# Kernel tuning notes

Measured on AMD Instinct MI355X. Metric: run time of the kernel, lower is better.

## Reference

```python
import jax, jax.numpy as jnp
import numpy as np

N = 50000
E = 600000
IN_C = 128
HID_C = 128
OUT_C = 128


def _glorot(key, shape):
    fan_in, fan_out = shape[0], shape[1]
    lim = np.sqrt(6.0 / (fan_in + fan_out))
    return jax.random.uniform(key, shape, jnp.float32, -lim, lim)


def setup_inputs() -> dict:
    key = jax.random.key(0)
    ks = jax.random.split(key, 10)
    x = jax.random.normal(ks[0], (N, IN_C), jnp.float32)
    edge_index = jax.random.randint(ks[1], (2, E), 0, N, jnp.int64)
    return {
        "x": x,
        "edge_index": edge_index,
        # SAGEConv1: lin_l (aggregated, with bias) and lin_r (root, no bias)
        "W1_l": _glorot(ks[2], (IN_C, HID_C)),
        "b1_l": jnp.zeros((HID_C,), jnp.float32),
        "W1_r": _glorot(ks[3], (IN_C, HID_C)),
        # SAGEConv2
        "W2_l": _glorot(ks[4], (HID_C, OUT_C)),
        "b2_l": jnp.zeros((OUT_C,), jnp.float32),
        "W2_r": _glorot(ks[5], (HID_C, OUT_C)),
        # final Linear(hidden+out -> out)
        "W_lin": _glorot(ks[6], (HID_C + OUT_C, OUT_C)),
        "b_lin": jnp.zeros((OUT_C,), jnp.float32),
    }


def _sage_conv(x, src, dst, W_l, b_l, W_r):
    # mean-aggregate source features onto destination nodes
    msg = x[src]                                   # [E, C] gather
    agg = jax.ops.segment_sum(msg, dst, num_segments=N)        # [N, C]
    cnt = jax.ops.segment_sum(jnp.ones((src.shape[0],), x.dtype), dst,
                              num_segments=N)                   # [N]
    mean = agg / jnp.maximum(cnt, 1.0)[:, None]
    return mean @ W_l + b_l + x @ W_r


def reference(x, edge_index, W1_l, b1_l, W1_r, W2_l, b2_l, W2_r, W_lin, b_lin):
    src, dst = edge_index[0], edge_index[1]
    x1 = jax.nn.relu(_sage_conv(x, src, dst, W1_l, b1_l, W1_r))   # [N, HID]
    x2 = jax.nn.relu(_sage_conv(x1, src, dst, W2_l, b2_l, W2_r))  # [N, OUT]
    return jnp.concatenate([x1, x2], axis=-1) @ W_lin + b_lin     # [N, OUT]
```

## Files before the change

### kernel.cpp

```cpp
#include <hip/hip_runtime.h>


typedef _Float16 f16;
typedef unsigned int u32;
typedef __attribute__((ext_vector_type(4))) _Float16 f16x4;
typedef __attribute__((ext_vector_type(8))) _Float16 f16x8;
typedef __attribute__((ext_vector_type(4))) float f32x4;

#define RNB 128

__global__ void prep_kernel(const float* __restrict__ x, f16* __restrict__ xh, int n4,
                            const int* __restrict__ ei, int* __restrict__ ghist, int E,
                            const float* __restrict__ W1l, const float* __restrict__ W1r,
                            const float* __restrict__ W2l, const float* __restrict__ W2r,
                            const float* __restrict__ Wlin, f16* __restrict__ wt,
                            int cb, int wb) {
  int b = blockIdx.x;
  if (b < cb) {
    int i = b * 256 + threadIdx.x;
    if (i < n4) {
      const float4 v = ((const float4*)x)[i];
      f16x4 h = { (f16)v.x, (f16)v.y, (f16)v.z, (f16)v.w };
      ((f16x4*)xh)[i] = h;
    }
  } else if (b < cb + wb) {
    int tid = (b - cb) * 256 + threadIdx.x;
    int w = tid >> 15, idx = tid & 32767;
    int j = idx & 7, n = (idx >> 3) & 127, chunk = idx >> 10;
    int k = chunk * 8 + j;
    float v;
    if (w == 0) v = (k < 128) ? W1l[k * 128 + n] : W1r[(k - 128) * 128 + n];
    else if (w == 1) v = (k < 128) ? W2l[k * 128 + n] : W2r[(k - 128) * 128 + n];
    else v = Wlin[k * 128 + n];
    wt[tid] = (f16)v;
  } else {
    __shared__ int h[256];
    int tid = threadIdx.x, rb = b - cb - wb;
    h[tid] = 0;
    __syncthreads();
    int per = (E + RNB - 1) / RNB;
    int s = rb * per, e = s + per; if (e > E) e = E;
    for (int i = s + tid; i < e; i += 256) atomicAdd(&h[ei[E + i] >> 8], 1);
    __syncthreads();
    ghist[tid * RNB + rb] = h[tid];
  }
}

__device__ inline int block_excl_scan256(int v, int* ws) {
  int lane = threadIdx.x & 63, w = threadIdx.x >> 6;
  int incl = v;
#pragma unroll
  for (int o = 1; o < 64; o <<= 1) {
    int u = __shfl_up(incl, o);
    if (lane >= o) incl += u;
  }
  if (lane == 63) ws[w] = incl;
  __syncthreads();
  int base = 0;
#pragma unroll
  for (int i = 0; i < 4; ++i) base += (i < w) ? ws[i] : 0;
  return base + incl - v;
}

__global__ void radix_scatter(const int* __restrict__ ei, const int* __restrict__ ghist,
                              u32* __restrict__ tmp, int E) {
  __shared__ int cur[256];
  __shared__ int ws[4];
  int tid = threadIdx.x, b = blockIdx.x;
  const int* row = ghist + tid * RNB;
  int part = 0, rest = 0;
  for (int i = 0; i < b; ++i) part += row[i];
  for (int i = b; i < RNB; ++i) rest += row[i];
  int total = part + rest;
  int excl = block_excl_scan256(total, ws);
  cur[tid] = excl + part;
  __syncthreads();
  int per = (E + RNB - 1) / RNB;
  int s = b * per, e = s + per; if (e > E) e = E;
  for (int i = s + tid; i < e; i += 256) {
    int d = ei[E + i], sr = ei[i];
    int pos = atomicAdd(&cur[d >> 8], 1);
    tmp[pos] = ((u32)sr << 8) | (u32)(d & 255);
  }
}

__global__ void radix_bucket(const u32* __restrict__ tmp, const int* __restrict__ ghist,
                             int* __restrict__ srcs, int* __restrict__ off,
                             int N, int E, int HB) {
  __shared__ int h[256], sc[256], cur[256];
  __shared__ int bsc[257];
  __shared__ int ws[4];
  int tid = threadIdx.x, hb = blockIdx.x;
  const int* row = ghist + tid * RNB;
  int total = 0;
#pragma unroll 4
  for (int i = 0; i < RNB; ++i) total += row[i];
  int excl = block_excl_scan256(total, ws);
  bsc[tid] = excl;
  if (tid == 255) bsc[256] = E;
  h[tid] = 0;
  __syncthreads();
  int start = bsc[hb];
  int end = bsc[hb + 1];
  for (int i = start + tid; i < end; i += 256) atomicAdd(&h[tmp[i] & 255u], 1);
  __syncthreads();
  sc[tid] = h[tid];
  __syncthreads();
  for (int o = 1; o < 256; o <<= 1) {
    int u = (tid >= o) ? sc[tid - o] : 0;
    __syncthreads();
    sc[tid] += u;
    __syncthreads();
  }
  int exclb = sc[tid] - h[tid];
  int v = (hb << 8) + tid;
  if (v < N) off[v] = start + exclb;
  if (hb == 0 && tid == 0) off[N] = E;
  cur[tid] = start + exclb;
  __syncthreads();
  for (int i = start + tid; i < end; i += 256) {
    u32 p = tmp[i];
    int pos = atomicAdd(&cur[p & 255u], 1);
    srcs[pos] = (int)(p >> 8);
  }
}

#define AGG_R 6
template <bool HEAD>
__global__ __launch_bounds__(256, 4) void fused_kernel(
    const f16* __restrict__ feat,
    const int* __restrict__ off, const int* __restrict__ srcs,
    const f16* __restrict__ WtA, const f16* __restrict__ WtB,
    const float* __restrict__ bA, const float* __restrict__ bB,
    void* __restrict__ outp, int n) {
  __shared__ f16 lds[16384];
  int tid = threadIdx.x;
  int wave = tid >> 6, lane = tid & 63;
  int sub = lane >> 4, n15 = lane & 15;
  int base = blockIdx.x * 32;

#pragma unroll
  for (int i = 0; i < 4; ++i)
    ((f16x8*)lds)[i * 256 + tid] = ((const f16x8*)WtA)[i * 256 + tid];

#pragma unroll 1
  for (int p = 0; p < 4; ++p) {
    int ln0 = p * 8 + wave * 2;
    int w0 = base + ln0, w1 = w0 + 1;
    bool a0 = w0 < n, a1 = w1 < n;
    int beg0 = a0 ? off[w0] : 0;
    int end0 = a0 ? off[w0 + 1] : 0;
    int beg1 = end0;
    int end1 = a1 ? off[w1 + 1] : end0;
    int deg0 = end0 - beg0, deg1 = end1 - beg1;

    int s0[AGG_R], s1[AGG_R];
    bool v0[AGG_R], v1[AGG_R];
#pragma unroll
    for (int k = 0; k < AGG_R; ++k) {
      int pp = 4 * k + sub;
      v0[k] = pp < deg0;  s0[k] = v0[k] ? srcs[beg0 + pp] : 0;
      v1[k] = pp < deg1;  s1[k] = v1[k] ? srcs[beg1 + pp] : 0;
    }
    f16x8 g0[AGG_R], g1[AGG_R];
#pragma unroll
    for (int k = 0; k < AGG_R; ++k) {
      if (v0[k]) g0[k] = *(const f16x8*)(feat + (size_t)s0[k] * 128 + n15 * 8);
      if (v1[k]) g1[k] = *(const f16x8*)(feat + (size_t)s1[k] * 128 + n15 * 8);
    }
    float acc0[8] = {}, acc1[8] = {};
#pragma unroll
    for (int k = 0; k < AGG_R; ++k) {
      if (v0[k]) {
#pragma unroll
        for (int j = 0; j < 8; ++j) acc0[j] += (float)g0[k][j];
      }
      if (v1[k]) {
#pragma unroll
        for (int j = 0; j < 8; ++j) acc1[j] += (float)g1[k][j];
      }
    }
    for (int e = beg0 + 4 * AGG_R; e < end0; e += 4) {
      if (sub < end0 - e) {
        int s = srcs[e + sub];
        f16x8 g = *(const f16x8*)(feat + (size_t)s * 128 + n15 * 8);
#pragma unroll
        for (int j = 0; j < 8; ++j) acc0[j] += (float)g[j];
      }
    }
    for (int e = beg1 + 4 * AGG_R; e < end1; e += 4) {
      if (sub < end1 - e) {
        int s = srcs[e + sub];
        f16x8 g = *(const f16x8*)(feat + (size_t)s * 128 + n15 * 8);
#pragma unroll
        for (int j = 0; j < 8; ++j) acc1[j] += (float)g[j];
      }
    }
#pragma unroll
    for (int j = 0; j < 8; ++j) {
      acc0[j] += __shfl_xor(acc0[j], 16);
      acc0[j] += __shfl_xor(acc0[j], 32);
      acc1[j] += __shfl_xor(acc1[j], 16);
      acc1[j] += __shfl_xor(acc1[j], 32);
    }
    if (sub == 0) {
      float inv = 1.0f / fmaxf((float)deg0, 1.0f);
      f16x8 o;
#pragma unroll
      for (int j = 0; j < 8; ++j) o[j] = (f16)(acc0[j] * inv);
      *(f16x8*)(lds + 8192 + ln0 * 128 + ((n15 ^ (ln0 & 15)) << 3)) = o;
    } else if (sub == 1) {
      float inv = 1.0f / fmaxf((float)deg1, 1.0f);
      int ln1 = ln0 + 1;
      f16x8 o;
#pragma unroll
      for (int j = 0; j < 8; ++j) o[j] = (f16)(acc1[j] * inv);
      *(f16x8*)(lds + 8192 + ln1 * 128 + ((n15 ^ (ln1 & 15)) << 3)) = o;
    }
  }
  __syncthreads();

  int rg = wave & 1, ch = wave >> 1;
  int rowl = rg * 16 + n15;
  int colb = ch * 64;

  f16x8 a[8];
#pragma unroll
  for (int kk = 0; kk < 4; ++kk)
    a[kk] = *(const f16x8*)(lds + 8192 + rowl * 128 + (((kk * 4 + sub) ^ n15) << 3));
  {
    int node = base + rowl; if (node >= n) node = n - 1;
    const f16* bp = feat + (size_t)node * 128 + sub * 8;
#pragma unroll
    for (int kk = 4; kk < 8; ++kk) a[kk] = *(const f16x8*)(bp + (kk - 4) * 32);
  }

  f32x4 acc[4] = {};
#pragma unroll
  for (int q = 0; q < 4; ++q) {
#pragma unroll
    for (int kk = 2 * q; kk < 2 * q + 2; ++kk)
#pragma unroll
      for (int t = 0; t < 4; ++t) {
        f16x8 bfr = ((const f16x8*)lds)[((kk * 4 + sub) & 7) * 128 + colb + t * 16 + n15];
        acc[t] = __builtin_amdgcn_mfma_f32_16x16x32_f16(a[kk], bfr, acc[t], 0, 0, 0);
      }
    if (q < 3) {
      __syncthreads();
#pragma unroll
      for (int i = 0; i < 4; ++i)
        ((f16x8*)lds)[i * 256 + tid] = ((const f16x8*)WtA)[(q + 1) * 1024 + i * 256 + tid];
      __syncthreads();
    }
  }

  if (!HEAD) {
#pragma unroll
    for (int t = 0; t < 4; ++t) {
      float bv = bA[colb + t * 16 + n15];
#pragma unroll
      for (int i = 0; i < 4; ++i) {
        int row = base + rg * 16 + sub * 4 + i;
        if (row < n) {
          float v = fmaxf(acc[t][i] + bv, 0.f);
          ((f16*)outp)[(size_t)row * 128 + colb + t * 16 + n15] = (f16)v;
        }
      }
    }
  } else {
    __syncthreads();
#pragma unroll
    for (int t = 0; t < 4; ++t) {
      float bv = bA[colb + t * 16 + n15];
      int col = colb + t * 16 + n15;
      int cchunk = col >> 3, coff = col & 7;
#pragma unroll
      for (int i = 0; i < 4; ++i) {
        int rw = rg * 16 + sub * 4 + i;
        float v = fmaxf(acc[t][i] + bv, 0.f);
        lds[12288 + rw * 128 + (((cchunk ^ (rw & 15)) << 3) | coff)] = (f16)v;
      }
    }
#pragma unroll
    for (int i = 0; i < 4; ++i)
      ((f16x8*)lds)[i * 256 + tid] = ((const f16x8*)WtB)[i * 256 + tid];
    __syncthreads();

    f16x8 a2[4];
#pragma unroll
    for (int kk2 = 0; kk2 < 4; ++kk2)
      a2[kk2] = *(const f16x8*)(lds + 12288 + rowl * 128 + (((kk2 * 4 + sub) ^ n15) << 3));

    f32x4 acc3[4] = {};
#pragma unroll
    for (int q = 0; q < 4; ++q) {
#pragma unroll
      for (int kk = 2 * q; kk < 2 * q + 2; ++kk)
#pragma unroll
        for (int t = 0; t < 4; ++t) {
          f16x8 bfr = ((const f16x8*)lds)[((kk * 4 + sub) & 7) * 128 + colb + t * 16 + n15];
          f16x8 av = (kk < 4) ? a[4 + kk] : a2[kk - 4];
          acc3[t] = __builtin_amdgcn_mfma_f32_16x16x32_f16(av, bfr, acc3[t], 0, 0, 0);
        }
      if (q < 3) {
        __syncthreads();
#pragma unroll
        for (int i = 0; i < 4; ++i)
          ((f16x8*)lds)[i * 256 + tid] = ((const f16x8*)WtB)[(q + 1) * 1024 + i * 256 + tid];
        __syncthreads();
      }
    }
#pragma unroll
    for (int t = 0; t < 4; ++t) {
      float bv = bB[colb + t * 16 + n15];
#pragma unroll
      for (int i = 0; i < 4; ++i) {
        int row = base + rg * 16 + sub * 4 + i;
        if (row < n)
          ((float*)outp)[(size_t)row * 128 + colb + t * 16 + n15] = acc3[t][i] + bv;
      }
    }
  }
}

extern "C" void kernel_launch(void* const* d_in, const int* in_sizes, int n_in,
                              void* d_out, int out_size, void* d_ws, size_t ws_size,
                              hipStream_t stream) {
  (void)n_in; (void)out_size; (void)ws_size;
  const float* x    = (const float*)d_in[0];
  const int*   ei   = (const int*)d_in[1];
  const float* W1l  = (const float*)d_in[2];
  const float* b1l  = (const float*)d_in[3];
  const float* W1r  = (const float*)d_in[4];
  const float* W2l  = (const float*)d_in[5];
  const float* b2l  = (const float*)d_in[6];
  const float* W2r  = (const float*)d_in[7];
  const float* Wlin = (const float*)d_in[8];
  const float* blin = (const float*)d_in[9];
  const int N = in_sizes[0] / 128;
  const int E = in_sizes[1] / 2;

  char* ws = (char*)d_ws;
  size_t o = 0;
  auto alloc = [&](size_t bytes) {
    char* p = ws + o;
    o = (o + bytes + 255) & ~(size_t)255;
    return p;
  };
  f16*  xh   = (f16*)alloc((size_t)N * 128 * 2);
  f16*  x1h  = (f16*)alloc((size_t)N * 128 * 2);
  f16*  wt   = (f16*)alloc((size_t)3 * 32768 * 2);
  int*  off  = (int*)alloc(((size_t)N + 1) * 4);
  int*  srcs = (int*)alloc((size_t)E * 4);
  u32*  tmp  = (u32*)alloc((size_t)E * 4);
  int*  ghist= (int*)alloc(256 * RNB * 4);
  f16* wt1 = wt, *wt2 = wt + 32768, *wt3 = wt + 65536;

  const int n4 = N * 128 / 4;
  const int cb = (n4 + 255) / 256;
  const int wb = (3 * 32768) / 256;
  const int HB = (N + 255) / 256;

  prep_kernel<<<cb + wb + RNB, 256, 0, stream>>>(x, xh, n4, ei, ghist, E,
                                                 W1l, W1r, W2l, W2r, Wlin, wt, cb, wb);
  radix_scatter<<<RNB, 256, 0, stream>>>(ei, ghist, tmp, E);
  radix_bucket<<<HB, 256, 0, stream>>>(tmp, ghist, srcs, off, N, E, HB);

  const int fusedBlocks = (N + 31) / 32;

  fused_kernel<false><<<fusedBlocks, 256, 0, stream>>>(
      xh, off, srcs, wt1, (const f16*)nullptr, b1l, (const float*)nullptr, x1h, N);
  fused_kernel<true><<<fusedBlocks, 256, 0, stream>>>(
      x1h, off, srcs, wt2, wt3, b2l, blin, d_out, N);
}
```

Measured before the change: 226.1 us.

## Halve weight LDS staging chunks and raise occupancy to eight blocks per CU

Weights are now staged into LDS in 8 chunks of 8KB instead of 4 chunks of 16KB. The shared array shrinks to 16KB for the non-head kernel and 24KB for the head kernel, and launch bounds are raised to 8 blocks per CU. The goal is more resident waves to hide the latency of the irregular neighbor gathers. In exchange, each GEMM does twice as many barrier/reload rounds, and tighter register limits may cause spills.

```diff
diff --git a/kernel.cpp b/kernel.cpp
--- a/kernel.cpp
+++ b/kernel.cpp
@@ -127,21 +127,20 @@
 
 #define AGG_R 6
 template <bool HEAD>
-__global__ __launch_bounds__(256, 4) void fused_kernel(
+__global__ __launch_bounds__(256, 8) void fused_kernel(
     const f16* __restrict__ feat,
     const int* __restrict__ off, const int* __restrict__ srcs,
     const f16* __restrict__ WtA, const f16* __restrict__ WtB,
     const float* __restrict__ bA, const float* __restrict__ bB,
     void* __restrict__ outp, int n) {
-  __shared__ f16 lds[16384];
+  __shared__ f16 lds[HEAD ? 12288 : 8192];
   int tid = threadIdx.x;
   int wave = tid >> 6, lane = tid & 63;
   int sub = lane >> 4, n15 = lane & 15;
   int base = blockIdx.x * 32;
 
-#pragma unroll
-  for (int i = 0; i < 4; ++i)
-    ((f16x8*)lds)[i * 256 + tid] = ((const f16x8*)WtA)[i * 256 + tid];
+  ((f16x8*)lds)[tid]       = ((const f16x8*)WtA)[tid];
+  ((f16x8*)lds)[256 + tid] = ((const f16x8*)WtA)[256 + tid];
 
 #pragma unroll 1
   for (int p = 0; p < 4; ++p) {
@@ -208,14 +207,14 @@
       f16x8 o;
 #pragma unroll
       for (int j = 0; j < 8; ++j) o[j] = (f16)(acc0[j] * inv);
-      *(f16x8*)(lds + 8192 + ln0 * 128 + ((n15 ^ (ln0 & 15)) << 3)) = o;
+      *(f16x8*)(lds + 4096 + ln0 * 128 + ((n15 ^ (ln0 & 15)) << 3)) = o;
     } else if (sub == 1) {
       float inv = 1.0f / fmaxf((float)deg1, 1.0f);
       int ln1 = ln0 + 1;
       f16x8 o;
 #pragma unroll
       for (int j = 0; j < 8; ++j) o[j] = (f16)(acc1[j] * inv);
-      *(f16x8*)(lds + 8192 + ln1 * 128 + ((n15 ^ (ln1 & 15)) << 3)) = o;
+      *(f16x8*)(lds + 4096 + ln1 * 128 + ((n15 ^ (ln1 & 15)) << 3)) = o;
     }
   }
   __syncthreads();
@@ -227,7 +226,7 @@
   f16x8 a[8];
 #pragma unroll
   for (int kk = 0; kk < 4; ++kk)
-    a[kk] = *(const f16x8*)(lds + 8192 + rowl * 128 + (((kk * 4 + sub) ^ n15) << 3));
+    a[kk] = *(const f16x8*)(lds + 4096 + rowl * 128 + (((kk * 4 + sub) ^ n15) << 3));
   {
     int node = base + rowl; if (node >= n) node = n - 1;
     const f16* bp = feat + (size_t)node * 128 + sub * 8;
@@ -237,20 +236,17 @@
 
   f32x4 acc[4] = {};
 #pragma unroll
-  for (int q = 0; q < 4; ++q) {
-#pragma unroll
-    for (int kk = 2 * q; kk < 2 * q + 2; ++kk)
-#pragma unroll
-      for (int t = 0; t < 4; ++t) {
-        f16x8 bfr = ((const f16x8*)lds)[((kk * 4 + sub) & 7) * 128 + colb + t * 16 + n15];
-        acc[t] = __builtin_amdgcn_mfma_f32_16x16x32_f16(a[kk], bfr, acc[t], 0, 0, 0);
-      }
-    if (q < 3) {
+  for (int q = 0; q < 8; ++q) {
+    if (q) {
       __syncthreads();
-#pragma unroll
-      for (int i = 0; i < 4; ++i)
-        ((f16x8*)lds)[i * 256 + tid] = ((const f16x8*)WtA)[(q + 1) * 1024 + i * 256 + tid];
+      ((f16x8*)lds)[tid]       = ((const f16x8*)WtA)[q * 512 + tid];
+      ((f16x8*)lds)[256 + tid] = ((const f16x8*)WtA)[q * 512 + 256 + tid];
       __syncthreads();
+    }
+#pragma unroll
+    for (int t = 0; t < 4; ++t) {
+      f16x8 bfr = ((const f16x8*)lds)[sub * 128 + colb + t * 16 + n15];
+      acc[t] = __builtin_amdgcn_mfma_f32_16x16x32_f16(a[q], bfr, acc[t], 0, 0, 0);
     }
   }
 
@@ -268,7 +264,6 @@
       }
     }
   } else {
-    __syncthreads();
 #pragma unroll
     for (int t = 0; t < 4; ++t) {
       float bv = bA[colb + t * 16 + n15];
@@ -278,36 +273,33 @@
       for (int i = 0; i < 4; ++i) {
         int rw = rg * 16 + sub * 4 + i;
         float v = fmaxf(acc[t][i] + bv, 0.f);
-        lds[12288 + rw * 128 + (((cchunk ^ (rw & 15)) << 3) | coff)] = (f16)v;
-      }
-    }
-#pragma unroll
-    for (int i = 0; i < 4; ++i)
-      ((f16x8*)lds)[i * 256 + tid] = ((const f16x8*)WtB)[i * 256 + tid];
+        lds[8192 + rw * 128 + (((cchunk ^ (rw & 15)) << 3) | coff)] = (f16)v;
+      }
+    }
+    __syncthreads();
+    ((f16x8*)lds)[tid]       = ((const f16x8*)WtB)[tid];
+    ((f16x8*)lds)[256 + tid] = ((const f16x8*)WtB)[256 + tid];
     __syncthreads();
 
     f16x8 a2[4];
 #pragma unroll
     for (int kk2 = 0; kk2 < 4; ++kk2)
-      a2[kk2] = *(const f16x8*)(lds + 12288 + rowl * 128 + (((kk2 * 4 + sub) ^ n15) << 3));
+      a2[kk2] = *(const f16x8*)(lds + 8192 + rowl * 128 + (((kk2 * 4 + sub) ^ n15) << 3));
 
     f32x4 acc3[4] = {};
 #pragma unroll
-    for (int q = 0; q < 4; ++q) {
-#pragma unroll
-      for (int kk = 2 * q; kk < 2 * q + 2; ++kk)
-#pragma unroll
-        for (int t = 0; t < 4; ++t) {
-          f16x8 bfr = ((const f16x8*)lds)[((kk * 4 + sub) & 7) * 128 + colb + t * 16 + n15];
-          f16x8 av = (kk < 4) ? a[4 + kk] : a2[kk - 4];
-          acc3[t] = __builtin_amdgcn_mfma_f32_16x16x32_f16(av, bfr, acc3[t], 0, 0, 0);
-        }
-      if (q < 3) {
+    for (int q = 0; q < 8; ++q) {
+      if (q) {
         __syncthreads();
-#pragma unroll
-        for (int i = 0; i < 4; ++i)
-          ((f16x8*)lds)[i * 256 + tid] = ((const f16x8*)WtB)[(q + 1) * 1024 + i * 256 + tid];
+        ((f16x8*)lds)[tid]       = ((const f16x8*)WtB)[q * 512 + tid];
+        ((f16x8*)lds)[256 + tid] = ((const f16x8*)WtB)[q * 512 + 256 + tid];
         __syncthreads();
+      }
+#pragma unroll
+      for (int t = 0; t < 4; ++t) {
+        f16x8 bfr = ((const f16x8*)lds)[sub * 128 + colb + t * 16 + n15];
+        f16x8 av = (q < 4) ? a[4 + q] : a2[q - 4];
+        acc3[t] = __builtin_amdgcn_mfma_f32_16x16x32_f16(av, bfr, acc3[t], 0, 0, 0);
       }
     }
 #pragma unroll
```

After: 290.0 us. +28.3%, slower.
